# Kernel tuning notes

Measured on AMD Instinct MI355X. Metric: run time of the kernel, lower is better.

## Reference

```python
import jax, jax.numpy as jnp
import numpy as np

B, L, D, V, K = 4, 2048, 1024, 32, 4096  # batch, seq, embedding_dim, vq_dim, num_embeddings


def setup_inputs() -> dict:
    key = jax.random.key(0)
    k0, k1, k2, k3 = jax.random.split(key, 4)
    h = jax.random.normal(k0, (B, L, D), jnp.float32)
    attn_mask = jnp.ones((B, L), jnp.float32)
    # proj: Linear(D -> V); proj_inv: Linear(V -> D)
    Wp = jax.random.normal(k1, (V, D), jnp.float32) / np.float32(np.sqrt(D))
    bp = jnp.zeros((V,), jnp.float32)
    Wpi = jax.random.normal(k2, (D, V), jnp.float32) / np.float32(np.sqrt(V))
    bpi = jnp.zeros((D,), jnp.float32)
    # embedding init uniform(-1/K, 1/K)
    emb = jax.random.uniform(k3, (K, V), jnp.float32, -1.0 / K, 1.0 / K)
    return {"h": h, "attn_mask": attn_mask, "Wp": Wp, "bp": bp,
            "Wpi": Wpi, "bpi": bpi, "emb": emb}


def reference(h, attn_mask, Wp, bp, Wpi, bpi, emb, temperature=1.0):
    # project + L2 normalize
    hp = jnp.einsum('bld,vd->blv', h, Wp) + bp            # [B,L,V]
    hp = hp / jnp.linalg.norm(hp, axis=-1, keepdims=True)
    # normalize codebook (in torch this is an in-place .data update)
    emb_n = emb / jnp.linalg.norm(emb, axis=-1, keepdims=True)  # [K,V]
    # squared euclidean distances hp vs codebook
    d = (jnp.sum(hp * hp, axis=-1, keepdims=True)
         + jnp.sum(emb_n * emb_n, axis=-1)
         - 2.0 * jnp.einsum('blv,kv->blk', hp, emb_n))    # [B,L,K]
    A = jax.nn.softmax(-d / temperature, axis=-1)         # [B,L,K]
    code = jnp.argmax(A, axis=-1)                         # [B,L]
    h_vq = jnp.einsum('blk,kv->blv', A, emb_n)            # train mode: A @ embedding
    # masked scatter into zeros is equivalent to masking out unselected positions
    m = (attn_mask == 1)
    quantized = jnp.where(m[..., None], h_vq, jnp.float32(0.0))
    vq_code = jnp.where(m, code, 0).astype(jnp.int32)
    quantized = jnp.einsum('blv,dv->bld', quantized, Wpi) + bpi
    vq_loss = jnp.float32(0.0)
    return quantized, vq_code, vq_loss
```

## Files before the change

kernel.cpp:

```cpp
#include <hip/hip_runtime.h>
#include <hip/hip_bf16.h>
#include <math.h>

#define NTOK 8192
#define DIM  1024
#define VDIM 32
#define KCODES 4096

#define SC 2.8853900817779268f

typedef __attribute__((ext_vector_type(8))) short short8;
typedef __attribute__((ext_vector_type(4))) float f32x4;

#define MFMA16(A,B,C) __builtin_amdgcn_mfma_f32_16x16x32_bf16(A, B, C, 0, 0, 0)

__device__ __forceinline__ unsigned short f2bf(float x) {
    unsigned u = __builtin_bit_cast(unsigned, x);
    u += 0x7FFF + ((u >> 16) & 1);
    return (unsigned short)(u >> 16);
}
__device__ __forceinline__ float bf2f(unsigned short b) {
    unsigned u = ((unsigned)b) << 16;
    return __builtin_bit_cast(float, u);
}
__device__ __forceinline__ float fexp2(float x) {
#if __has_builtin(__builtin_amdgcn_exp2f)
    return __builtin_amdgcn_exp2f(x);
#else
    return __expf(0.6931471805599453f * x);
#endif
}

struct U4 { unsigned x, y, z, w; };

__device__ __forceinline__ void split8(const float* p, short8* H, short8* L) {
    unsigned hh[4], ll[4];
    #pragma unroll
    for (int i = 0; i < 4; ++i) {
        unsigned short a = f2bf(p[2 * i]);
        unsigned short b = f2bf(p[2 * i + 1]);
        hh[i] = (unsigned)a | ((unsigned)b << 16);
        unsigned short la = f2bf(p[2 * i] - bf2f(a));
        unsigned short lb = f2bf(p[2 * i + 1] - bf2f(b));
        ll[i] = (unsigned)la | ((unsigned)lb << 16);
    }
    U4 uh = {hh[0], hh[1], hh[2], hh[3]};
    U4 ul = {ll[0], ll[1], ll[2], ll[3]};
    *H = __builtin_bit_cast(short8, uh);
    *L = __builtin_bit_cast(short8, ul);
}

__device__ __forceinline__ short8 pack8(const float* p) {
    unsigned u[8];
    #pragma unroll
    for (int j = 0; j < 8; ++j) u[j] = __builtin_bit_cast(unsigned, p[j]) + 0x8000u;
    U4 uh;
    uh.x = __builtin_amdgcn_perm(u[1], u[0], 0x07060302);
    uh.y = __builtin_amdgcn_perm(u[3], u[2], 0x07060302);
    uh.z = __builtin_amdgcn_perm(u[5], u[4], 0x07060302);
    uh.w = __builtin_amdgcn_perm(u[7], u[6], 0x07060302);
    return __builtin_bit_cast(short8, uh);
}

#define OFS_E_HI   0
#define OFS_E_LO   131072
#define OFS_ET_HI  262144
#define OFS_WP_HI  393216
#define OFS_WP_LO  425984
#define OFS_WPI_HI 458752
#define OFS_WPI_LO 491520
#define OFS_HP_HI  524288
#define OFS_HP_LO  786432
#define F32_BASE   1048576
#define NSPLIT 8
#define FOFS_HVP 0
#define FOFS_LP  2097152
#define FOFS_AMP 2162688
#define FOFS_AIP 2228224

__global__ __launch_bounds__(256) void k_prep(const float* __restrict__ emb,
                                              const float* __restrict__ Wp,
                                              const float* __restrict__ Wpi,
                                              unsigned short* __restrict__ W,
                                              float* __restrict__ loss_out) {
    __shared__ __align__(16) unsigned short Th[32][72];
    int bid = blockIdx.x, tid = threadIdx.x;
    if (bid < 64) {
        int cb = bid * 64;
        int c = tid >> 2, s = tid & 3;
        const float* src = emb + (size_t)(cb + c) * VDIM + s * 8;
        float4 a = *(const float4*)src;
        float4 b = *(const float4*)(src + 4);
        float ps = a.x*a.x + a.y*a.y + a.z*a.z + a.w*a.w
                 + b.x*b.x + b.y*b.y + b.z*b.z + b.w*b.w;
        ps += __shfl_xor(ps, 1);
        ps += __shfl_xor(ps, 2);
        float inv = 1.0f / sqrtf(ps);
        float vals[8] = {a.x*inv, a.y*inv, a.z*inv, a.w*inv,
                         b.x*inv, b.y*inv, b.z*inv, b.w*inv};
        short8 H, L;
        split8(vals, &H, &L);
        *(short8*)(W + OFS_E_HI + (size_t)(cb + c) * VDIM + s * 8) = H;
        *(short8*)(W + OFS_E_LO + (size_t)(cb + c) * VDIM + s * 8) = L;
        #pragma unroll
        for (int j = 0; j < 8; ++j) Th[s * 8 + j][c] = f2bf(vals[j]);
        __syncthreads();
        int row = tid >> 3, seg = tid & 7;
        *(short8*)(W + OFS_ET_HI + (size_t)row * KCODES + cb + seg * 8) =
            *(const short8*)&Th[row][seg * 8];
        if (bid == 0 && tid == 0) loss_out[0] = 0.0f;
    } else if (bid < 80) {
        int i0 = (bid - 64) * 2048 + tid * 8;
        float4 a = *(const float4*)(Wp + i0);
        float4 b = *(const float4*)(Wp + i0 + 4);
        float vals[8] = {a.x, a.y, a.z, a.w, b.x, b.y, b.z, b.w};
        short8 H, L;
        split8(vals, &H, &L);
        *(short8*)(W + OFS_WP_HI + i0) = H;
        *(short8*)(W + OFS_WP_LO + i0) = L;
    } else {
        int i0 = (bid - 80) * 2048 + tid * 8;
        float4 a = *(const float4*)(Wpi + i0);
        float4 b = *(const float4*)(Wpi + i0 + 4);
        float vals[8] = {a.x, a.y, a.z, a.w, b.x, b.y, b.z, b.w};
        short8 H, L;
        split8(vals, &H, &L);
        *(short8*)(W + OFS_WPI_HI + i0) = H;
        *(short8*)(W + OFS_WPI_LO + i0) = L;
    }
}

__global__ __launch_bounds__(256) void k_proj(const float* __restrict__ h,
                                              const unsigned short* __restrict__ W,
                                              const float* __restrict__ bp,
                                              unsigned short* __restrict__ hp_hi,
                                              unsigned short* __restrict__ hp_lo) {
    __shared__ __align__(16) float red[4][16][36];
    const unsigned short* Wp_hi = W + OFS_WP_HI;
    const unsigned short* Wp_lo = W + OFS_WP_LO;
    int tid = threadIdx.x;
    int w = tid >> 6, l = tid & 63, q = l >> 4, m = l & 15;
    int tok0 = blockIdx.x * 16;
    const f32x4 zero4 = {0.f, 0.f, 0.f, 0.f};
    f32x4 acc0 = zero4, acc1 = zero4;
    const float* hb = h + (size_t)(tok0 + m) * DIM + w * 256 + q * 8;
    const unsigned short* w0h = Wp_hi + (size_t)m * DIM + w * 256 + q * 8;
    const unsigned short* w0l = Wp_lo + (size_t)m * DIM + w * 256 + q * 8;
    const unsigned short* w1h = w0h + (size_t)16 * DIM;
    const unsigned short* w1l = w0l + (size_t)16 * DIM;
    #pragma unroll
    for (int c = 0; c < 8; ++c) {
        float4 a = *(const float4*)(hb + c * 32);
        float4 b = *(const float4*)(hb + c * 32 + 4);
        float va[8] = {a.x, a.y, a.z, a.w, b.x, b.y, b.z, b.w};
        short8 Bh, Bl;
        split8(va, &Bh, &Bl);
        short8 A0h = *(const short8*)(w0h + c * 32);
        short8 A0l = *(const short8*)(w0l + c * 32);
        short8 A1h = *(const short8*)(w1h + c * 32);
        short8 A1l = *(const short8*)(w1l + c * 32);
        acc0 = MFMA16(A0l, Bl, acc0); acc0 = MFMA16(A0l, Bh, acc0);
        acc0 = MFMA16(A0h, Bl, acc0); acc0 = MFMA16(A0h, Bh, acc0);
        acc1 = MFMA16(A1l, Bl, acc1); acc1 = MFMA16(A1l, Bh, acc1);
        acc1 = MFMA16(A1h, Bl, acc1); acc1 = MFMA16(A1h, Bh, acc1);
    }
    *(f32x4*)&red[w][m][4 * q]      = acc0;
    *(f32x4*)&red[w][m][16 + 4 * q] = acc1;
    __syncthreads();
    #pragma unroll
    for (int half = 0; half < 2; ++half) {
        int t = (tid >> 5) + half * 8, v = tid & 31;
        float s = bp[v];
        #pragma unroll
        for (int j = 0; j < 4; ++j) s += red[j][t][v];
        float sq = s * s;
        #pragma unroll
        for (int off = 1; off < 32; off <<= 1) sq += __shfl_xor(sq, off);
        float nv = s * (SC / sqrtf(sq));
        unsigned short hb2 = f2bf(nv);
        size_t idx = (size_t)(tok0 + t) * VDIM + v;
        hp_hi[idx] = hb2;
        hp_lo[idx] = f2bf(nv - bf2f(hb2));
    }
}

__global__ __launch_bounds__(256, 4) void k_vq(const unsigned short* __restrict__ W,
                                               float* __restrict__ hvp,
                                               float* __restrict__ lp,
                                               float* __restrict__ amp,
                                               int* __restrict__ aip) {
    __shared__ __align__(16) float red2[2][64][36];
    __shared__ float lred[4][4][16];
    __shared__ float amred[4][4][16];
    __shared__ int   aired[4][4][16];

    const unsigned short* E_hi  = W + OFS_E_HI;
    const unsigned short* E_lo  = W + OFS_E_LO;
    const unsigned short* Et_hi = W + OFS_ET_HI;
    const unsigned short* hp_hi = W + OFS_HP_HI;
    const unsigned short* hp_lo = W + OFS_HP_LO;

    int tid = threadIdx.x;
    int w = tid >> 6, l = tid & 63, q = l >> 4, m = l & 15;
    int tg = blockIdx.x >> 3, sp = blockIdx.x & 7;
    int tok0 = tg * 64;
    int cb0 = sp * 512 + w * 128;
    int sig = ((m & 12) << 1) | (m & 3);
    const f32x4 zero4 = {0.f, 0.f, 0.f, 0.f};

    short8 hph[4], hpl[4];
    #pragma unroll
    for (int t = 0; t < 4; ++t) {
        size_t hidx = (size_t)(tok0 + t * 16 + m) * VDIM + q * 8;
        hph[t] = *(const short8*)(hp_hi + hidx);
        hpl[t] = *(const short8*)(hp_lo + hidx);
    }

    f32x4 hv[4][2];
    #pragma unroll
    for (int t = 0; t < 4; ++t) { hv[t][0] = zero4; hv[t][1] = zero4; }
    float ls[4] = {0.f, 0.f, 0.f, 0.f};
    float am[4] = {-1e30f, -1e30f, -1e30f, -1e30f};
    int   ai[4] = {0, 0, 0, 0};

    #pragma unroll 1
    for (int c = 0; c < 4; ++c) {
        int cbase = cb0 + c * 32;
        size_t e0 = (size_t)(cbase + sig) * VDIM + q * 8;
        short8 E0h = *(const short8*)(E_hi + e0);
        short8 E0l = *(const short8*)(E_lo + e0);
        short8 E1h = *(const short8*)(E_hi + e0 + 4 * VDIM);
        short8 E1l = *(const short8*)(E_lo + e0 + 4 * VDIM);
        size_t t0 = (size_t)sig * KCODES + cbase + q * 8;
        short8 T0h = *(const short8*)(Et_hi + t0);
        short8 T1h = *(const short8*)(Et_hi + t0 + (size_t)4 * KCODES);
        int lbase = cbase + 8 * q;
        #pragma unroll
        for (int t = 0; t < 4; ++t) {
            f32x4 s0 = MFMA16(E0l, hpl[t], zero4);
            s0 = MFMA16(E0l, hph[t], s0);
            s0 = MFMA16(E0h, hpl[t], s0);
            s0 = MFMA16(E0h, hph[t], s0);
            f32x4 s1 = MFMA16(E1l, hpl[t], zero4);
            s1 = MFMA16(E1l, hph[t], s1);
            s1 = MFMA16(E1h, hpl[t], s1);
            s1 = MFMA16(E1h, hph[t], s1);
            float p[8];
            #pragma unroll
            for (int r = 0; r < 4; ++r) {
                float sv = s0[r];
                if (sv > am[t]) { am[t] = sv; ai[t] = lbase + r; }
                p[r] = fexp2(sv);
                sv = s1[r];
                if (sv > am[t]) { am[t] = sv; ai[t] = lbase + 4 + r; }
                p[4 + r] = fexp2(sv);
            }
            ls[t] += ((p[0] + p[1]) + (p[2] + p[3])) + ((p[4] + p[5]) + (p[6] + p[7]));
            short8 Ph = pack8(p);
            hv[t][0] = MFMA16(T0h, Ph, hv[t][0]);
            hv[t][1] = MFMA16(T1h, Ph, hv[t][1]);
        }
    }

    #pragma unroll
    for (int t = 0; t < 4; ++t) {
        #pragma unroll
        for (int off = 16; off <= 32; off <<= 1) {
            ls[t] += __shfl_xor(ls[t], off);
            float a2 = __shfl_xor(am[t], off);
            int   i2 = __shfl_xor(ai[t], off);
            if (a2 > am[t] || (a2 == am[t] && i2 < ai[t])) { am[t] = a2; ai[t] = i2; }
        }
    }
    if (q == 0) {
        #pragma unroll
        for (int t = 0; t < 4; ++t) {
            lred[w][t][m] = ls[t]; amred[w][t][m] = am[t]; aired[w][t][m] = ai[t];
        }
    }
    if (w < 2) {
        #pragma unroll
        for (int t = 0; t < 4; ++t) {
            *(f32x4*)&red2[w][t * 16 + m][8 * q]     = hv[t][0];
            *(f32x4*)&red2[w][t * 16 + m][8 * q + 4] = hv[t][1];
        }
    }
    __syncthreads();
    if (w >= 2) {
        #pragma unroll
        for (int t = 0; t < 4; ++t) {
            f32x4* d0 = (f32x4*)&red2[w - 2][t * 16 + m][8 * q];
            f32x4* d1 = (f32x4*)&red2[w - 2][t * 16 + m][8 * q + 4];
            *d0 = *d0 + hv[t][0];
            *d1 = *d1 + hv[t][1];
        }
    }
    __syncthreads();
    if (tid < 64) {
        int t = tid >> 4, tl = tid & 15;
        float L = 0.f, A = -1e30f;
        int I = 0x7fffffff;
        #pragma unroll
        for (int ww = 0; ww < 4; ++ww) {
            L += lred[ww][t][tl];
            float a2 = amred[ww][t][tl];
            int   i2 = aired[ww][t][tl];
            if (a2 > A || (a2 == A && i2 < I)) { A = a2; I = i2; }
        }
        size_t gi = (size_t)sp * NTOK + tok0 + tid;
        lp[gi] = L; amp[gi] = A; aip[gi] = I;
    }
    #pragma unroll
    for (int it = 0; it < 2; ++it) {
        int idx = it * 256 + tid;
        int tl = idx >> 3, v0 = (idx & 7) * 4;
        f32x4 xs = *(const f32x4*)&red2[0][tl][v0];
        f32x4 ys = *(const f32x4*)&red2[1][tl][v0];
        f32x4 sum = xs + ys;
        *(f32x4*)(hvp + ((size_t)sp * NTOK + tok0 + tl) * VDIM + v0) = sum;
    }
}

__global__ __launch_bounds__(256) void k_out(const unsigned short* __restrict__ W,
                                             const float* __restrict__ mask,
                                             const float* __restrict__ bpi,
                                             const float* __restrict__ hvp,
                                             const float* __restrict__ lp,
                                             const float* __restrict__ amp,
                                             const int* __restrict__ aip,
                                             float* __restrict__ out,
                                             float* __restrict__ code_out) {
    __shared__ float invl[16];
    __shared__ __align__(16) unsigned short hvh[16][40];
    __shared__ __align__(16) unsigned short hvl[16][40];
    const unsigned short* Wpi_hi = W + OFS_WPI_HI;
    const unsigned short* Wpi_lo = W + OFS_WPI_LO;
    int tid = threadIdx.x;
    int tok0 = blockIdx.x * 16;
    const f32x4 zero4 = {0.f, 0.f, 0.f, 0.f};

    if (tid < 16) {
        int tk = tok0 + tid;
        float L = 0.f, A = -1e30f;
        int I = 0x7fffffff;
        #pragma unroll
        for (int sp = 0; sp < NSPLIT; ++sp) {
            size_t gi = (size_t)sp * NTOK + tk;
            L += lp[gi];
            float a2 = amp[gi];
            int   i2 = aip[gi];
            if (a2 > A || (a2 == A && i2 < I)) { A = a2; I = i2; }
        }
        bool on = (mask[tk] == 1.0f);
        code_out[tk] = on ? (float)I : 0.0f;
        invl[tid] = on ? (1.0f / L) : 0.0f;
    }
    __syncthreads();
    #pragma unroll
    for (int it = 0; it < 2; ++it) {
        int idx = it * 256 + tid;
        int t = idx >> 5, v = idx & 31;
        float x = 0.f;
        #pragma unroll
        for (int sp = 0; sp < NSPLIT; ++sp)
            x += hvp[((size_t)sp * NTOK + tok0 + t) * VDIM + v];
        x *= invl[t];
        unsigned short hb = f2bf(x);
        hvh[t][v] = hb;
        hvl[t][v] = f2bf(x - bf2f(hb));
    }
    __syncthreads();
    int w = tid >> 6, l = tid & 63, q = l >> 4, m = l & 15;
    short8 gh = *(const short8*)&hvh[m][q * 8];
    short8 gl = *(const short8*)&hvl[m][q * 8];
    #pragma unroll
    for (int dt = 0; dt < 16; ++dt) {
        int dbase = w * 256 + dt * 16;
        short8 Ah = *(const short8*)(Wpi_hi + (size_t)(dbase + m) * VDIM + q * 8);
        short8 Al = *(const short8*)(Wpi_lo + (size_t)(dbase + m) * VDIM + q * 8);
        f32x4 o = MFMA16(Al, gh, zero4);
        o = MFMA16(Ah, gl, o);
        o = MFMA16(Ah, gh, o);
        float4 bias = *(const float4*)(bpi + dbase + 4 * q);
        float4 r0 = make_float4(o[0] + bias.x, o[1] + bias.y,
                                o[2] + bias.z, o[3] + bias.w);
        *(float4*)(out + (size_t)(tok0 + m) * DIM + dbase + 4 * q) = r0;
    }
}

extern "C" void kernel_launch(void* const* d_in, const int* in_sizes, int n_in,
                              void* d_out, int out_size, void* d_ws, size_t ws_size,
                              hipStream_t stream) {
    const float* h    = (const float*)d_in[0];
    const float* mask = (const float*)d_in[1];
    const float* Wp   = (const float*)d_in[2];
    const float* bp   = (const float*)d_in[3];
    const float* Wpi  = (const float*)d_in[4];
    const float* bpi  = (const float*)d_in[5];
    const float* emb  = (const float*)d_in[6];
    float* out = (float*)d_out;

    unsigned short* W = (unsigned short*)d_ws;
    unsigned short* hp_hi = W + OFS_HP_HI;
    unsigned short* hp_lo = W + OFS_HP_LO;
    float* fbase = (float*)(W + F32_BASE);
    float* hvp = fbase + FOFS_HVP;
    float* lpp = fbase + FOFS_LP;
    float* ampp = fbase + FOFS_AMP;
    int*   aipp = (int*)(fbase + FOFS_AIP);

    float* code_out = out + (size_t)NTOK * DIM;
    float* loss_out = code_out + NTOK;

    hipLaunchKernelGGL(k_prep, dim3(96),   dim3(256), 0, stream, emb, Wp, Wpi, W, loss_out);
    hipLaunchKernelGGL(k_proj, dim3(512),  dim3(256), 0, stream, h, W, bp, hp_hi, hp_lo);
    hipLaunchKernelGGL(k_vq,   dim3(1024), dim3(256), 0, stream, W, hvp, lpp, ampp, aipp);
    hipLaunchKernelGGL(k_out,  dim3(512),  dim3(256), 0, stream, W, mask, bpi, hvp, lpp, ampp, aipp, out, code_out);
}
```

Before: 142.8 us.

## Give each wave its own tokens in k_vq and drop cross-wave LDS reduction

```diff
diff --git a/kernel.cpp b/kernel.cpp
--- a/kernel.cpp
+++ b/kernel.cpp
@@ -184,16 +184,11 @@
     }
 }
 
-__global__ __launch_bounds__(256, 4) void k_vq(const unsigned short* __restrict__ W,
-                                               float* __restrict__ hvp,
-                                               float* __restrict__ lp,
-                                               float* __restrict__ amp,
-                                               int* __restrict__ aip) {
-    __shared__ __align__(16) float red2[2][64][36];
-    __shared__ float lred[4][4][16];
-    __shared__ float amred[4][4][16];
-    __shared__ int   aired[4][4][16];
-
+__global__ __launch_bounds__(256) void k_vq(const unsigned short* __restrict__ W,
+                                            float* __restrict__ hvp,
+                                            float* __restrict__ lp,
+                                            float* __restrict__ amp,
+                                            int* __restrict__ aip) {
     const unsigned short* E_hi  = W + OFS_E_HI;
     const unsigned short* E_lo  = W + OFS_E_LO;
     const unsigned short* Et_hi = W + OFS_ET_HI;
@@ -203,28 +198,21 @@
     int tid = threadIdx.x;
     int w = tid >> 6, l = tid & 63, q = l >> 4, m = l & 15;
     int tg = blockIdx.x >> 3, sp = blockIdx.x & 7;
-    int tok0 = tg * 64;
-    int cb0 = sp * 512 + w * 128;
+    int tok0 = tg * 64 + w * 16;
+    int cb0 = sp * 512;
     int sig = ((m & 12) << 1) | (m & 3);
     const f32x4 zero4 = {0.f, 0.f, 0.f, 0.f};
 
-    short8 hph[4], hpl[4];
-    #pragma unroll
-    for (int t = 0; t < 4; ++t) {
-        size_t hidx = (size_t)(tok0 + t * 16 + m) * VDIM + q * 8;
-        hph[t] = *(const short8*)(hp_hi + hidx);
-        hpl[t] = *(const short8*)(hp_lo + hidx);
-    }
-
-    f32x4 hv[4][2];
-    #pragma unroll
-    for (int t = 0; t < 4; ++t) { hv[t][0] = zero4; hv[t][1] = zero4; }
-    float ls[4] = {0.f, 0.f, 0.f, 0.f};
-    float am[4] = {-1e30f, -1e30f, -1e30f, -1e30f};
-    int   ai[4] = {0, 0, 0, 0};
-
-    #pragma unroll 1
-    for (int c = 0; c < 4; ++c) {
+    size_t hidx = (size_t)(tok0 + m) * VDIM + q * 8;
+    short8 hph = *(const short8*)(hp_hi + hidx);
+    short8 hpl = *(const short8*)(hp_lo + hidx);
+
+    f32x4 hv0 = zero4, hv1 = zero4;
+    float ls = 0.f, am = -1e30f;
+    int ai = 0;
+
+    #pragma unroll 2
+    for (int c = 0; c < 16; ++c) {
         int cbase = cb0 + c * 32;
         size_t e0 = (size_t)(cbase + sig) * VDIM + q * 8;
         short8 E0h = *(const short8*)(E_hi + e0);
@@ -234,91 +222,47 @@
         size_t t0 = (size_t)sig * KCODES + cbase + q * 8;
         short8 T0h = *(const short8*)(Et_hi + t0);
         short8 T1h = *(const short8*)(Et_hi + t0 + (size_t)4 * KCODES);
+
+        f32x4 s0 = MFMA16(E0l, hpl, zero4);
+        s0 = MFMA16(E0l, hph, s0);
+        s0 = MFMA16(E0h, hpl, s0);
+        s0 = MFMA16(E0h, hph, s0);
+        f32x4 s1 = MFMA16(E1l, hpl, zero4);
+        s1 = MFMA16(E1l, hph, s1);
+        s1 = MFMA16(E1h, hpl, s1);
+        s1 = MFMA16(E1h, hph, s1);
+
+        float p[8];
         int lbase = cbase + 8 * q;
         #pragma unroll
-        for (int t = 0; t < 4; ++t) {
-            f32x4 s0 = MFMA16(E0l, hpl[t], zero4);
-            s0 = MFMA16(E0l, hph[t], s0);
-            s0 = MFMA16(E0h, hpl[t], s0);
-            s0 = MFMA16(E0h, hph[t], s0);
-            f32x4 s1 = MFMA16(E1l, hpl[t], zero4);
-            s1 = MFMA16(E1l, hph[t], s1);
-            s1 = MFMA16(E1h, hpl[t], s1);
-            s1 = MFMA16(E1h, hph[t], s1);
-            float p[8];
-            #pragma unroll
-            for (int r = 0; r < 4; ++r) {
-                float sv = s0[r];
-                if (sv > am[t]) { am[t] = sv; ai[t] = lbase + r; }
-                p[r] = fexp2(sv);
-                sv = s1[r];
-                if (sv > am[t]) { am[t] = sv; ai[t] = lbase + 4 + r; }
-                p[4 + r] = fexp2(sv);
-            }
-            ls[t] += ((p[0] + p[1]) + (p[2] + p[3])) + ((p[4] + p[5]) + (p[6] + p[7]));
-            short8 Ph = pack8(p);
-            hv[t][0] = MFMA16(T0h, Ph, hv[t][0]);
-            hv[t][1] = MFMA16(T1h, Ph, hv[t][1]);
+        for (int r = 0; r < 4; ++r) {
+            float sv = s0[r];
+            if (sv > am) { am = sv; ai = lbase + r; }
+            p[r] = fexp2(sv);
+            sv = s1[r];
+            if (sv > am) { am = sv; ai = lbase + 4 + r; }
+            p[4 + r] = fexp2(sv);
         }
-    }
-
-    #pragma unroll
-    for (int t = 0; t < 4; ++t) {
-        #pragma unroll
-        for (int off = 16; off <= 32; off <<= 1) {
-            ls[t] += __shfl_xor(ls[t], off);
-            float a2 = __shfl_xor(am[t], off);
-            int   i2 = __shfl_xor(ai[t], off);
-            if (a2 > am[t] || (a2 == am[t] && i2 < ai[t])) { am[t] = a2; ai[t] = i2; }
-        }
-    }
+        ls += ((p[0] + p[1]) + (p[2] + p[3])) + ((p[4] + p[5]) + (p[6] + p[7]));
+        short8 Ph = pack8(p);
+        hv0 = MFMA16(T0h, Ph, hv0);
+        hv1 = MFMA16(T1h, Ph, hv1);
+    }
+
+    #pragma unroll
+    for (int off = 16; off <= 32; off <<= 1) {
+        ls += __shfl_xor(ls, off);
+        float a2 = __shfl_xor(am, off);
+        int   i2 = __shfl_xor(ai, off);
+        if (a2 > am || (a2 == am && i2 < ai)) { am = a2; ai = i2; }
+    }
+    size_t gtok = (size_t)sp * NTOK + tok0;
     if (q == 0) {
-        #pragma unroll
-        for (int t = 0; t < 4; ++t) {
-            lred[w][t][m] = ls[t]; amred[w][t][m] = am[t]; aired[w][t][m] = ai[t];
-        }
-    }
-    if (w < 2) {
-        #pragma unroll
-        for (int t = 0; t < 4; ++t) {
-            *(f32x4*)&red2[w][t * 16 + m][8 * q]     = hv[t][0];
-            *(f32x4*)&red2[w][t * 16 + m][8 * q + 4] = hv[t][1];
-        }
-    }
-    __syncthreads();
-    if (w >= 2) {
-        #pragma unroll
-        for (int t = 0; t < 4; ++t) {
-            f32x4* d0 = (f32x4*)&red2[w - 2][t * 16 + m][8 * q];
-            f32x4* d1 = (f32x4*)&red2[w - 2][t * 16 + m][8 * q + 4];
-            *d0 = *d0 + hv[t][0];
-            *d1 = *d1 + hv[t][1];
-        }
-    }
-    __syncthreads();
-    if (tid < 64) {
-        int t = tid >> 4, tl = tid & 15;
-        float L = 0.f, A = -1e30f;
-        int I = 0x7fffffff;
-        #pragma unroll
-        for (int ww = 0; ww < 4; ++ww) {
-            L += lred[ww][t][tl];
-            float a2 = amred[ww][t][tl];
-            int   i2 = aired[ww][t][tl];
-            if (a2 > A || (a2 == A && i2 < I)) { A = a2; I = i2; }
-        }
-        size_t gi = (size_t)sp * NTOK + tok0 + tid;
-        lp[gi] = L; amp[gi] = A; aip[gi] = I;
-    }
-    #pragma unroll
-    for (int it = 0; it < 2; ++it) {
-        int idx = it * 256 + tid;
-        int tl = idx >> 3, v0 = (idx & 7) * 4;
-        f32x4 xs = *(const f32x4*)&red2[0][tl][v0];
-        f32x4 ys = *(const f32x4*)&red2[1][tl][v0];
-        f32x4 sum = xs + ys;
-        *(f32x4*)(hvp + ((size_t)sp * NTOK + tok0 + tl) * VDIM + v0) = sum;
-    }
+        lp[gtok + m] = ls; amp[gtok + m] = am; aip[gtok + m] = ai;
+    }
+    float* dst = hvp + (gtok + m) * VDIM;
+    *(f32x4*)(dst + 8 * q)     = hv0;
+    *(f32x4*)(dst + 8 * q + 4) = hv1;
 }
 
 __global__ __launch_bounds__(256) void k_out(const unsigned short* __restrict__ W,
```

Measured after the change: 151.8 us. +6.3%, slower.
